# Performance work log

Measured on AMD Instinct MI355X. Metric: run time of the kernel, lower is better.

Reference implementation:

```python
import jax, jax.numpy as jnp
import numpy as np

N, DIM, K = 262144, 64, 1024

def setup_inputs() -> dict:
    key = jax.random.key(0)
    k1, k2 = jax.random.split(key)
    x = jax.random.normal(k1, (N, DIM), dtype=jnp.float32)
    embed = jax.random.normal(k2, (K, DIM), dtype=jnp.float32)
    return {"x": x, "embed": embed}

def reference(x, embed):
    distances = (jnp.sum(x * x, axis=-1, keepdims=True)
                 - 2.0 * (x @ embed.T)
                 + jnp.sum(embed * embed, axis=-1))  # [N, K]
    idx = jnp.argmin(distances, axis=-1)  # [N]
    # dequantize: embedding lookup
    out = embed[idx]  # [N, DIM]
    return out
```

## Files before the change

kernel.cpp:

```cpp
#include <hip/hip_runtime.h>


#define VQ_N 262144
#define VQ_DIM 64
#define VQ_K 1024
#define NT 64
#define TCH 256
#define FLAG_EPS 1.2e-2f

typedef short short8 __attribute__((ext_vector_type(8)));
typedef float f32x4 __attribute__((ext_vector_type(4)));

#define WS_BFRAG 0
#define WS_E2    (256*1024)
#define WS_E2P   (260*1024)
#define WS_NEEDED (264*1024)

static __device__ __forceinline__ unsigned short f2bf_rtne(float f) {
    unsigned u = __float_as_uint(f);
    unsigned r = u + 0x7FFFu + ((u >> 16) & 1u);
    return (unsigned short)(r >> 16);
}
static __device__ __forceinline__ float bf2f(unsigned short h) {
    return __uint_as_float(((unsigned)h) << 16);
}

__global__ void vq_prep(const float* __restrict__ embed, unsigned char* ws) {
    int t = blockIdx.x * 256 + threadIdx.x;
    if (t < NT * TCH) {
        int ct = t >> 8;
        int c = t & 255;
        int arr = c >> 7;
        int kc = (c >> 6) & 1;
        int l = c & 63;
        int code = ct * 16 + (l & 15);
        int kbase = kc * 32 + ((l >> 4) << 3);
        const float* ep = embed + (size_t)code * VQ_DIM + kbase;
        short8 pack;
#pragma unroll
        for (int j = 0; j < 8; ++j) {
            float v = ep[j];
            unsigned short h = f2bf_rtne(v);
            pack[j] = arr ? (short)f2bf_rtne(v - bf2f(h)) : (short)h;
        }
        ((short8*)(ws + WS_BFRAG))[t] = pack;
    } else if (t < NT * TCH + VQ_K) {
        int code = t - NT * TCH;
        const float* ep = embed + (size_t)code * VQ_DIM;
        float a0 = 0, a1 = 0, a2 = 0, a3 = 0;
#pragma unroll
        for (int j = 0; j < VQ_DIM; j += 4) {
            a0 = fmaf(ep[j], ep[j], a0);
            a1 = fmaf(ep[j + 1], ep[j + 1], a1);
            a2 = fmaf(ep[j + 2], ep[j + 2], a2);
            a3 = fmaf(ep[j + 3], ep[j + 3], a3);
        }
        float e2 = (a0 + a1) + (a2 + a3);
        ((float*)(ws + WS_E2))[code] = e2;
        ((float*)(ws + WS_E2P))[code] = e2 + 256.0f;
    }
}

__global__ __launch_bounds__(64, 4)
void vq_stage1(const float* __restrict__ x, const float* __restrict__ embed,
               unsigned char* ws, float* __restrict__ out) {
    const int lane = threadIdx.x;
    const int gwave = blockIdx.x;
    const int R0 = gwave * 32;
    const int g = lane >> 4;
    const int res = lane & 15;
    const int khalf = g << 3;

    const short8* bsrc = (const short8*)(ws + WS_BFRAG);
    const float* e2g = (const float*)(ws + WS_E2);
    const float* e2p = (const float*)(ws + WS_E2P);

    short8 ah00, ah01, al00, al01, ah10, ah11, al10, al11;
#define MAKE_A(ROW, KC, AH, AL)                                             \
    {                                                                       \
        const float4* p4 = (const float4*)(x + (size_t)(ROW) * VQ_DIM +     \
                                           (KC) * 32 + khalf);              \
        float4 v0 = p4[0], v1 = p4[1];                                      \
        float q0 = -2.0f * v0.x, q1 = -2.0f * v0.y, q2 = -2.0f * v0.z,      \
              q3 = -2.0f * v0.w, q4 = -2.0f * v1.x, q5 = -2.0f * v1.y,      \
              q6 = -2.0f * v1.z, q7 = -2.0f * v1.w;                         \
        unsigned short h0 = f2bf_rtne(q0), h1 = f2bf_rtne(q1),              \
                       h2 = f2bf_rtne(q2), h3 = f2bf_rtne(q3),              \
                       h4 = f2bf_rtne(q4), h5 = f2bf_rtne(q5),              \
                       h6 = f2bf_rtne(q6), h7 = f2bf_rtne(q7);              \
        AH[0] = (short)h0; AH[1] = (short)h1; AH[2] = (short)h2;            \
        AH[3] = (short)h3; AH[4] = (short)h4; AH[5] = (short)h5;            \
        AH[6] = (short)h6; AH[7] = (short)h7;                               \
        AL[0] = (short)f2bf_rtne(q0 - bf2f(h0));                            \
        AL[1] = (short)f2bf_rtne(q1 - bf2f(h1));                            \
        AL[2] = (short)f2bf_rtne(q2 - bf2f(h2));                            \
        AL[3] = (short)f2bf_rtne(q3 - bf2f(h3));                            \
        AL[4] = (short)f2bf_rtne(q4 - bf2f(h4));                            \
        AL[5] = (short)f2bf_rtne(q5 - bf2f(h5));                            \
        AL[6] = (short)f2bf_rtne(q6 - bf2f(h6));                            \
        AL[7] = (short)f2bf_rtne(q7 - bf2f(h7));                            \
    }
    const int row0 = R0 + res;
    const int row1 = row0 + 16;
    MAKE_A(row0, 0, ah00, al00)
    MAKE_A(row0, 1, ah01, al01)
    MAKE_A(row1, 0, ah10, al10)
    MAKE_A(row1, 1, ah11, al11)
#undef MAKE_A

    unsigned m1k0[4], m2k0[4], m1k1[4], m2k1[4];
#pragma unroll
    for (int r = 0; r < 4; ++r) {
        m1k0[r] = 0xFFFFFFFFu; m2k0[r] = 0xFFFFFFFFu;
        m1k1[r] = 0xFFFFFFFFu; m2k1[r] = 0xFFFFFFFFu;
    }

#pragma unroll 2
    for (int ct = 0; ct < NT; ++ct) {
        const short8* bt = bsrc + (size_t)ct * TCH;
        short8 bh0 = bt[lane];
        short8 bh1 = bt[64 + lane];
        short8 bl0 = bt[128 + lane];
        short8 bl1 = bt[192 + lane];
        float e2c = e2p[ct * 16 + res];
        unsigned ctu = (unsigned)ct;

        f32x4 acc0 = {e2c, e2c, e2c, e2c};
        acc0 = __builtin_amdgcn_mfma_f32_16x16x32_bf16(al00, bh0, acc0, 0, 0, 0);
        acc0 = __builtin_amdgcn_mfma_f32_16x16x32_bf16(al01, bh1, acc0, 0, 0, 0);
        acc0 = __builtin_amdgcn_mfma_f32_16x16x32_bf16(ah00, bl0, acc0, 0, 0, 0);
        acc0 = __builtin_amdgcn_mfma_f32_16x16x32_bf16(ah01, bl1, acc0, 0, 0, 0);
        acc0 = __builtin_amdgcn_mfma_f32_16x16x32_bf16(ah00, bh0, acc0, 0, 0, 0);
        acc0 = __builtin_amdgcn_mfma_f32_16x16x32_bf16(ah01, bh1, acc0, 0, 0, 0);

        f32x4 acc1 = {e2c, e2c, e2c, e2c};
        acc1 = __builtin_amdgcn_mfma_f32_16x16x32_bf16(al10, bh0, acc1, 0, 0, 0);
        acc1 = __builtin_amdgcn_mfma_f32_16x16x32_bf16(al11, bh1, acc1, 0, 0, 0);
        acc1 = __builtin_amdgcn_mfma_f32_16x16x32_bf16(ah10, bl0, acc1, 0, 0, 0);
        acc1 = __builtin_amdgcn_mfma_f32_16x16x32_bf16(ah11, bl1, acc1, 0, 0, 0);
        acc1 = __builtin_amdgcn_mfma_f32_16x16x32_bf16(ah10, bh0, acc1, 0, 0, 0);
        acc1 = __builtin_amdgcn_mfma_f32_16x16x32_bf16(ah11, bh1, acc1, 0, 0, 0);

#pragma unroll
        for (int r = 0; r < 4; ++r) {
            unsigned key = (__float_as_uint(acc0[r]) & 0xFFFFFFC0u) | ctu;
            unsigned t1 = m1k0[r] > key ? m1k0[r] : key;
            m2k0[r] = m2k0[r] < t1 ? m2k0[r] : t1;
            m1k0[r] = m1k0[r] < key ? m1k0[r] : key;
        }
#pragma unroll
        for (int r = 0; r < 4; ++r) {
            unsigned key = (__float_as_uint(acc1[r]) & 0xFFFFFFC0u) | ctu;
            unsigned t1 = m1k1[r] > key ? m1k1[r] : key;
            m2k1[r] = m2k1[r] < t1 ? m2k1[r] : t1;
            m1k1[r] = m1k1[r] < key ? m1k1[r] : key;
        }
    }

    unsigned res0[4], res1[4];
#pragma unroll
    for (int r = 0; r < 4; ++r) { res0[r] = (unsigned)res; res1[r] = res0[r]; }
#define RED_STEP(M1, M2, RES, m)                                                      \
    {                                                                                 \
        _Pragma("unroll")                                                             \
        for (int r = 0; r < 4; ++r) {                                                 \
            unsigned ok = (unsigned)__shfl_xor((int)M1[r], m);                        \
            unsigned ok2 = (unsigned)__shfl_xor((int)M2[r], m);                       \
            unsigned orr = (unsigned)__shfl_xor((int)RES[r], m);                      \
            unsigned t1 = M1[r] > ok ? M1[r] : ok;                                    \
            unsigned c2 = ok2 < t1 ? ok2 : t1;                                        \
            M2[r] = M2[r] < c2 ? M2[r] : c2;                                          \
            bool take = (ok < M1[r]) || (ok == M1[r] && orr < RES[r]);                \
            if (take) { M1[r] = ok; RES[r] = orr; }                                   \
        }                                                                             \
    }
#pragma unroll
    for (int m = 1; m <= 8; m <<= 1) {
        RED_STEP(m1k0, m2k0, res0, m)
        RED_STEP(m1k1, m2k1, res1, m)
    }
#undef RED_STEP

    int code0[4], code1[4];
    unsigned fmask = 0;
#pragma unroll
    for (int r = 0; r < 4; ++r) {
        code0[r] = (int)((m1k0[r] & 63u) * 16u + res0[r]);
        code1[r] = (int)((m1k1[r] & 63u) * 16u + res1[r]);
        float s1a = __uint_as_float(m1k0[r] & 0xFFFFFFC0u);
        float s2a = __uint_as_float(m2k0[r] & 0xFFFFFFC0u);
        if (s2a - s1a < FLAG_EPS) fmask |= 1u << (4 * g + r);
        float s1b = __uint_as_float(m1k1[r] & 0xFFFFFFC0u);
        float s2b = __uint_as_float(m2k1[r] & 0xFFFFFFC0u);
        if (s2b - s1b < FLAG_EPS) fmask |= 1u << (16 + 4 * g + r);
    }
    fmask |= (unsigned)__shfl_xor((int)fmask, 16);
    fmask |= (unsigned)__shfl_xor((int)fmask, 32);
    unsigned wmask = fmask;

    {
        const int q = lane >> 1;
        const int setq = q >> 4;
        const int gq = (q & 15) >> 2;
        const int rq = q & 3;
        const int src = gq << 4;
        int a0 = __shfl(code0[0], src), a1 = __shfl(code0[1], src);
        int a2 = __shfl(code0[2], src), a3 = __shfl(code0[3], src);
        int b0 = __shfl(code1[0], src), b1 = __shfl(code1[1], src);
        int b2 = __shfl(code1[2], src), b3 = __shfl(code1[3], src);
        int cs0 = (rq == 0) ? a0 : (rq == 1) ? a1 : (rq == 2) ? a2 : a3;
        int cs1 = (rq == 0) ? b0 : (rq == 1) ? b1 : (rq == 2) ? b2 : b3;
        int my = setq ? cs1 : cs0;
        const float4* ep = (const float4*)(embed + (size_t)my * VQ_DIM) + (lane & 1) * 8;
        float4* op = (float4*)(out + (size_t)(R0 + q) * VQ_DIM) + (lane & 1) * 8;
#pragma unroll
        for (int j = 0; j < 8; ++j) op[j] = ep[j];
    }

    while (wmask) {
        int b = __ffs(wmask) - 1;
        wmask &= wmask - 1;
        int row = R0 + b;
        const float* xr = x + (size_t)row * VQ_DIM;
        float best = __builtin_inff();
        int bi = VQ_K;
        for (int t = 0; t < VQ_K / 64; ++t) {
            int c = t * 64 + lane;
            const float* ep2 = embed + (size_t)c * VQ_DIM;
            float a0 = 0, a1 = 0, a2 = 0, a3 = 0;
#pragma unroll
            for (int j = 0; j < VQ_DIM; j += 4) {
                a0 = fmaf(xr[j], ep2[j], a0);
                a1 = fmaf(xr[j + 1], ep2[j + 1], a1);
                a2 = fmaf(xr[j + 2], ep2[j + 2], a2);
                a3 = fmaf(xr[j + 3], ep2[j + 3], a3);
            }
            float dot = (a0 + a1) + (a2 + a3);
            float s = fmaf(-2.0f, dot, e2g[c]);
            if (s < best || (s == best && c < bi)) { best = s; bi = c; }
        }
#pragma unroll
        for (int m = 1; m <= 32; m <<= 1) {
            float ob = __shfl_xor(best, m);
            int oi = __shfl_xor(bi, m);
            if (ob < best || (ob == best && oi < bi)) { best = ob; bi = oi; }
        }
        out[(size_t)row * VQ_DIM + lane] = embed[(size_t)bi * VQ_DIM + lane];
    }
}

__global__ __launch_bounds__(256, 4)
void vq_fallback(const float* __restrict__ x, const float* __restrict__ embed,
                 float* __restrict__ out) {
    __shared__ float e2s[VQ_K];
    const int tid = threadIdx.x;
    for (int c = tid; c < VQ_K; c += 256) {
        const float4* ep = (const float4*)(embed + c * VQ_DIM);
        float s = 0.0f;
#pragma unroll
        for (int j = 0; j < VQ_DIM / 4; ++j) {
            float4 v = ep[j];
            s = fmaf(v.x, v.x, s); s = fmaf(v.y, v.y, s);
            s = fmaf(v.z, v.z, s); s = fmaf(v.w, v.w, s);
        }
        e2s[c] = s;
    }
    __syncthreads();
    const int row = blockIdx.x * 256 + tid;
    float xr[VQ_DIM];
    const float4* xp = (const float4*)(x + (size_t)row * VQ_DIM);
#pragma unroll
    for (int j = 0; j < VQ_DIM / 4; ++j) {
        float4 v = xp[j];
        xr[4 * j] = v.x; xr[4 * j + 1] = v.y; xr[4 * j + 2] = v.z; xr[4 * j + 3] = v.w;
    }
    float best = __builtin_inff();
    int bidx = 0;
    for (int c = 0; c < VQ_K; ++c) {
        const float4* ep = (const float4*)(embed + c * VQ_DIM);
        float a0 = 0, a1 = 0, a2 = 0, a3 = 0;
#pragma unroll
        for (int j = 0; j < VQ_DIM / 4; ++j) {
            float4 v = ep[j];
            a0 = fmaf(xr[4 * j], v.x, a0);
            a1 = fmaf(xr[4 * j + 1], v.y, a1);
            a2 = fmaf(xr[4 * j + 2], v.z, a2);
            a3 = fmaf(xr[4 * j + 3], v.w, a3);
        }
        float score = fmaf(-2.0f, (a0 + a1) + (a2 + a3), e2s[c]);
        if (score < best) { best = score; bidx = c; }
    }
    const float4* bp = (const float4*)(embed + (size_t)bidx * VQ_DIM);
    float4* op = (float4*)(out + (size_t)row * VQ_DIM);
#pragma unroll
    for (int j = 0; j < VQ_DIM / 4; ++j) op[j] = bp[j];
}

extern "C" void kernel_launch(void* const* d_in, const int* in_sizes, int n_in,
                              void* d_out, int out_size, void* d_ws, size_t ws_size,
                              hipStream_t stream) {
    const float* x = (const float*)d_in[0];
    const float* embed = (const float*)d_in[1];
    float* out = (float*)d_out;
    if (ws_size < WS_NEEDED) {
        hipLaunchKernelGGL(vq_fallback, dim3(VQ_N / 256), dim3(256), 0, stream, x, embed, out);
        return;
    }
    unsigned char* ws = (unsigned char*)d_ws;
    hipLaunchKernelGGL(vq_prep, dim3(68), dim3(256), 0, stream, embed, ws);
    hipLaunchKernelGGL(vq_stage1, dim3(VQ_N / 32), dim3(64), 0, stream, x, embed, ws, out);
}
```

Before: 176.5 us.

## Pack four waves per block, split bf16 hi/lo codebook, use med3 for top-2

The main kernel now launches 256-thread blocks holding four independent waves instead of one-wave blocks, which cuts the block count and changes occupancy and scheduling. The codebook bf16 hi and lo fragments are stored in two separate arrays rather than interleaved per tile. The second-min update in the top-2 tracking becomes a single v_med3_u32 inline-asm instruction. The exact fallback loop for flagged rows switches to float4 loads. Together these aim to reduce per-iteration ALU work and launch overhead, at the cost of new register-pressure limits from the larger block under the launch bounds.

```diff
diff --git a/kernel.cpp b/kernel.cpp
--- a/kernel.cpp
+++ b/kernel.cpp
@@ -5,13 +5,14 @@
 #define VQ_DIM 64
 #define VQ_K 1024
 #define NT 64
-#define TCH 256
+#define TCH 128
 #define FLAG_EPS 1.2e-2f
 
 typedef short short8 __attribute__((ext_vector_type(8)));
 typedef float f32x4 __attribute__((ext_vector_type(4)));
 
-#define WS_BFRAG 0
+#define WS_BH    0
+#define WS_BL    (128*1024)
 #define WS_E2    (256*1024)
 #define WS_E2P   (260*1024)
 #define WS_NEEDED (264*1024)
@@ -24,13 +25,18 @@
 static __device__ __forceinline__ float bf2f(unsigned short h) {
     return __uint_as_float(((unsigned)h) << 16);
 }
+static __device__ __forceinline__ unsigned med3u(unsigned a, unsigned b, unsigned c) {
+    unsigned d;
+    asm("v_med3_u32 %0, %1, %2, %3" : "=v"(d) : "v"(a), "v"(b), "v"(c));
+    return d;
+}
 
 __global__ void vq_prep(const float* __restrict__ embed, unsigned char* ws) {
     int t = blockIdx.x * 256 + threadIdx.x;
-    if (t < NT * TCH) {
-        int ct = t >> 8;
-        int c = t & 255;
-        int arr = c >> 7;
+    if (t < 16384) {
+        int arr = t >> 13;
+        int c = t & 8191;
+        int ct = c >> 7;
         int kc = (c >> 6) & 1;
         int l = c & 63;
         int code = ct * 16 + (l & 15);
@@ -43,9 +49,9 @@
             unsigned short h = f2bf_rtne(v);
             pack[j] = arr ? (short)f2bf_rtne(v - bf2f(h)) : (short)h;
         }
-        ((short8*)(ws + WS_BFRAG))[t] = pack;
-    } else if (t < NT * TCH + VQ_K) {
-        int code = t - NT * TCH;
+        ((short8*)(ws + (arr ? WS_BL : WS_BH)))[c] = pack;
+    } else if (t < 16384 + VQ_K) {
+        int code = t - 16384;
         const float* ep = embed + (size_t)code * VQ_DIM;
         float a0 = 0, a1 = 0, a2 = 0, a3 = 0;
 #pragma unroll
@@ -61,17 +67,20 @@
     }
 }
 
-__global__ __launch_bounds__(64, 4)
+__global__ __launch_bounds__(256, 4)
 void vq_stage1(const float* __restrict__ x, const float* __restrict__ embed,
                unsigned char* ws, float* __restrict__ out) {
-    const int lane = threadIdx.x;
-    const int gwave = blockIdx.x;
+    const int tid = threadIdx.x;
+    const int lane = tid & 63;
+    const int wave = tid >> 6;
+    const int gwave = blockIdx.x * 4 + wave;
     const int R0 = gwave * 32;
     const int g = lane >> 4;
     const int res = lane & 15;
     const int khalf = g << 3;
 
-    const short8* bsrc = (const short8*)(ws + WS_BFRAG);
+    const short8* bh = (const short8*)(ws + WS_BH);
+    const short8* bl = (const short8*)(ws + WS_BL);
     const float* e2g = (const float*)(ws + WS_E2);
     const float* e2p = (const float*)(ws + WS_E2P);
 
@@ -117,11 +126,12 @@
 
 #pragma unroll 2
     for (int ct = 0; ct < NT; ++ct) {
-        const short8* bt = bsrc + (size_t)ct * TCH;
-        short8 bh0 = bt[lane];
-        short8 bh1 = bt[64 + lane];
-        short8 bl0 = bt[128 + lane];
-        short8 bl1 = bt[192 + lane];
+        const short8* bht = bh + (size_t)ct * TCH;
+        const short8* blt = bl + (size_t)ct * TCH;
+        short8 bh0 = bht[lane];
+        short8 bh1 = bht[64 + lane];
+        short8 bl0 = blt[lane];
+        short8 bl1 = blt[64 + lane];
         float e2c = e2p[ct * 16 + res];
         unsigned ctu = (unsigned)ct;
 
@@ -144,15 +154,13 @@
 #pragma unroll
         for (int r = 0; r < 4; ++r) {
             unsigned key = (__float_as_uint(acc0[r]) & 0xFFFFFFC0u) | ctu;
-            unsigned t1 = m1k0[r] > key ? m1k0[r] : key;
-            m2k0[r] = m2k0[r] < t1 ? m2k0[r] : t1;
+            m2k0[r] = med3u(m1k0[r], m2k0[r], key);
             m1k0[r] = m1k0[r] < key ? m1k0[r] : key;
         }
 #pragma unroll
         for (int r = 0; r < 4; ++r) {
             unsigned key = (__float_as_uint(acc1[r]) & 0xFFFFFFC0u) | ctu;
-            unsigned t1 = m1k1[r] > key ? m1k1[r] : key;
-            m2k1[r] = m2k1[r] < t1 ? m2k1[r] : t1;
+            m2k1[r] = med3u(m1k1[r], m2k1[r], key);
             m1k1[r] = m1k1[r] < key ? m1k1[r] : key;
         }
     }
@@ -221,19 +229,21 @@
         int b = __ffs(wmask) - 1;
         wmask &= wmask - 1;
         int row = R0 + b;
-        const float* xr = x + (size_t)row * VQ_DIM;
+        const float4* xr4 = (const float4*)(x + (size_t)row * VQ_DIM);
         float best = __builtin_inff();
         int bi = VQ_K;
         for (int t = 0; t < VQ_K / 64; ++t) {
             int c = t * 64 + lane;
-            const float* ep2 = embed + (size_t)c * VQ_DIM;
+            const float4* ep4 = (const float4*)(embed + (size_t)c * VQ_DIM);
             float a0 = 0, a1 = 0, a2 = 0, a3 = 0;
 #pragma unroll
-            for (int j = 0; j < VQ_DIM; j += 4) {
-                a0 = fmaf(xr[j], ep2[j], a0);
-                a1 = fmaf(xr[j + 1], ep2[j + 1], a1);
-                a2 = fmaf(xr[j + 2], ep2[j + 2], a2);
-                a3 = fmaf(xr[j + 3], ep2[j + 3], a3);
+            for (int j = 0; j < VQ_DIM / 4; ++j) {
+                float4 xv = xr4[j];
+                float4 ev = ep4[j];
+                a0 = fmaf(xv.x, ev.x, a0);
+                a1 = fmaf(xv.y, ev.y, a1);
+                a2 = fmaf(xv.z, ev.z, a2);
+                a3 = fmaf(xv.w, ev.w, a3);
             }
             float dot = (a0 + a1) + (a2 + a3);
             float s = fmaf(-2.0f, dot, e2g[c]);
@@ -307,6 +317,6 @@
         return;
     }
     unsigned char* ws = (unsigned char*)d_ws;
-    hipLaunchKernelGGL(vq_prep, dim3(68), dim3(256), 0, stream, embed, ws);
-    hipLaunchKernelGGL(vq_stage1, dim3(VQ_N / 32), dim3(64), 0, stream, x, embed, ws, out);
-}
+    hipLaunchKernelGGL(vq_prep, dim3(70), dim3(256), 0, stream, embed, ws);
+    hipLaunchKernelGGL(vq_stage1, dim3(VQ_N / 128), dim3(256), 0, stream, x, embed, ws, out);
+}
```

Result: faster. 170.7 us (median of 2 runs) (-3.3%).
